# Performance work log

Hardware: AMD Instinct MI355X
Metric: run time of the kernel (lower is better)

Reference implementation:

```python
import jax, jax.numpy as jnp
import numpy as np
import math

B, S, D, H = 2, 2048, 1024, 16
HD = D // H  # head dim = 64


def setup_inputs() -> dict:
    key = jax.random.key(0)
    ks = jax.random.split(key, 8)
    scale = 1.0 / math.sqrt(D)
    return {
        "x": jax.random.normal(ks[0], (B, S, D), dtype=jnp.float32),
        "mask": jax.random.randint(ks[1], (B, S, S), 0, 2).astype(bool),
        "Wq": jax.random.normal(ks[2], (D, D), dtype=jnp.float32) * scale,
        "bq": jax.random.normal(ks[3], (D,), dtype=jnp.float32) * 0.01,
        "Wk": jax.random.normal(ks[4], (D, D), dtype=jnp.float32) * scale,
        "bk": jax.random.normal(ks[5], (D,), dtype=jnp.float32) * 0.01,
        "Wv": jax.random.normal(ks[6], (D, D), dtype=jnp.float32) * scale,
        "bv": jax.random.normal(ks[7], (D,), dtype=jnp.float32) * 0.01,
    }


def reference(x, mask, Wq, bq, Wk, bk, Wv, bv):
    # Linear projections (weights stored as [in, out])
    q = x @ Wq + bq  # [B,S,D]
    k = x @ Wk + bk
    v = x @ Wv + bv
    # split heads -> [B,H,S,HD]
    q = q.reshape(B, S, H, HD).transpose(0, 2, 1, 3)
    k = k.reshape(B, S, H, HD).transpose(0, 2, 1, 3)
    v = v.reshape(B, S, H, HD).transpose(0, 2, 1, 3)
    scores = jnp.einsum("bhqd,bhkd->bhqk", q, k) / jnp.sqrt(jnp.float32(HD))
    # Faithful to the source: masked_fill_(mask, -inf) is immediately
    # overwritten by masked_fill_(mask, 0), so masked positions end up 0
    # BEFORE the softmax (a quirk of the original module).
    scores = jnp.where(mask[:, None, :, :], 0.0, scores)
    attn = jax.nn.softmax(scores, axis=-1)  # dropout=0.0 (eval)
    out = jnp.einsum("bhqk,bhkd->bhqd", attn, v)
    return out.transpose(0, 2, 1, 3).reshape(B, S, D)
```

## Files before the change

kernel.cpp:

```cpp
#include <hip/hip_runtime.h>
#include <cstdint>
#include <cstddef>

static constexpr int B_ = 2, S_ = 2048, D_ = 1024, H_ = 16, HD_ = 64;

typedef float f32x4 __attribute__((ext_vector_type(4)));
typedef short bf16x8 __attribute__((ext_vector_type(8)));

__device__ __forceinline__ unsigned short f2bf(float f) {
    union { float f; unsigned int u; } v; v.f = f;
    unsigned int r = v.u + 0x7FFFu + ((v.u >> 16) & 1u);
    return (unsigned short)(r >> 16);
}
__device__ __forceinline__ float bf2f(unsigned short h) {
    union { unsigned int u; float f; } v; v.u = ((unsigned int)h) << 16;
    return v.f;
}

__global__ __launch_bounds__(256)
void cast_x(const float* __restrict__ x, unsigned short* __restrict__ o) {
    size_t i = ((size_t)blockIdx.x * 256 + threadIdx.x) * 8;
    float4 a = *(const float4*)(x + i);
    float4 c = *(const float4*)(x + i + 4);
    uint4 r;
    r.x = (unsigned)f2bf(a.x) | ((unsigned)f2bf(a.y) << 16);
    r.y = (unsigned)f2bf(a.z) | ((unsigned)f2bf(a.w) << 16);
    r.z = (unsigned)f2bf(c.x) | ((unsigned)f2bf(c.y) << 16);
    r.w = (unsigned)f2bf(c.z) | ((unsigned)f2bf(c.w) << 16);
    *(uint4*)(o + i) = r;
}

__global__ __launch_bounds__(256)
void transpose_w(const float* __restrict__ Wq, const float* __restrict__ Wk,
                 const float* __restrict__ Wv, unsigned short* __restrict__ wt) {
    const int mat = blockIdx.z;
    const float* __restrict__ W = (mat == 0) ? Wq : (mat == 1) ? Wk : Wv;
    unsigned short* __restrict__ o = wt + (size_t)mat * D_ * D_;
    const int n0 = blockIdx.x * 64, k0 = blockIdx.y * 64;
    __shared__ unsigned short Ts[64][72];
    const int t = threadIdx.x;
    {
        const int nl = t & 63, kb = t >> 6;
        #pragma unroll
        for (int i = 0; i < 16; ++i) {
            int k = kb + i * 4;
            Ts[nl][k] = f2bf(W[(size_t)(k0 + k) * D_ + n0 + nl]);
        }
    }
    __syncthreads();
    {
        const int kl = t & 63, nb = t >> 6;
        #pragma unroll
        for (int i = 0; i < 16; ++i) {
            int n = nb + i * 4;
            o[(size_t)(n0 + n) * D_ + k0 + kl] = Ts[n][kl];
        }
    }
}

__global__ __launch_bounds__(256)
void qkv_gemm(const unsigned short* __restrict__ xb, const unsigned short* __restrict__ wt,
              const float* __restrict__ bq, const float* __restrict__ bk,
              const float* __restrict__ bv,
              unsigned short* __restrict__ qo, unsigned short* __restrict__ ko,
              unsigned short* __restrict__ vo) {
    const int bx = blockIdx.x;
    const int by = blockIdx.y;
    const int mat = bx >> 3;
    const int ncol0 = (bx & 7) * 128;
    const float* __restrict__ bias = (mat == 0) ? bq : (mat == 1) ? bk : bv;
    unsigned short* __restrict__ O = (mat == 0) ? qo : (mat == 1) ? ko : vo;
    const unsigned short* __restrict__ Wm = wt + (size_t)mat * D_ * D_;

    __shared__ unsigned short As[128][40];
    __shared__ unsigned short Bs[128][40];

    const int t = threadIdx.x;
    const int w = t >> 6, lane = t & 63;
    const int l15 = lane & 15, quad = lane >> 4;
    const int mw = (w >> 1) * 64, nw = (w & 1) * 64;
    const int rowBase = by * 128;

    f32x4 acc[4][4] = {};

    for (int kt = 0; kt < D_; kt += 32) {
        __syncthreads();
        #pragma unroll
        for (int i = 0; i < 2; ++i) {
            int c = t + i * 256;
            int r = c >> 2, q = c & 3;
            *(uint4*)&As[r][q * 8] =
                *(const uint4*)(xb + (size_t)(rowBase + r) * D_ + kt + q * 8);
            *(uint4*)&Bs[r][q * 8] =
                *(const uint4*)(Wm + (size_t)(ncol0 + r) * D_ + kt + q * 8);
        }
        __syncthreads();

        bf16x8 a[4], b[4];
        #pragma unroll
        for (int i = 0; i < 4; ++i)
            a[i] = *(const bf16x8*)&As[mw + i * 16 + l15][quad * 8];
        #pragma unroll
        for (int j = 0; j < 4; ++j)
            b[j] = *(const bf16x8*)&Bs[nw + j * 16 + l15][quad * 8];
        #pragma unroll
        for (int i = 0; i < 4; ++i)
            #pragma unroll
            for (int j = 0; j < 4; ++j)
                acc[i][j] = __builtin_amdgcn_mfma_f32_16x16x32_bf16(a[i], b[j], acc[i][j], 0, 0, 0);
    }

    #pragma unroll
    for (int j = 0; j < 4; ++j) {
        const int col = ncol0 + nw + j * 16 + l15;
        const float bb = bias[col];
        #pragma unroll
        for (int i = 0; i < 4; ++i) {
            #pragma unroll
            for (int r = 0; r < 4; ++r) {
                const int m = rowBase + mw + i * 16 + quad * 4 + r;
                O[(size_t)m * D_ + col] = f2bf(acc[i][j][r] + bb);
            }
        }
    }
}

__global__ __launch_bounds__(256)
void attn_mfma(const unsigned short* __restrict__ qmat,
               const unsigned short* __restrict__ kmat,
               const unsigned short* __restrict__ vmat,
               const int* __restrict__ mask, float* __restrict__ out) {
    const int h = blockIdx.x, qt = blockIdx.y, b = blockIdx.z;
    const int t = threadIdx.x, w = t >> 6, lane = t & 63;
    const int l15 = lane & 15, quad = lane >> 4;
    const int q0 = qt * 128;

    __shared__ unsigned short Qs[128][72];
    __shared__ unsigned short Ks[64][72];
    __shared__ unsigned short Vt[64][72];
    __shared__ unsigned short Ps[128][72];

    const size_t bh = (size_t)b * S_ * D_ + (size_t)h * HD_;
    const unsigned short* __restrict__ qp = qmat + bh;
    const unsigned short* __restrict__ kp = kmat + bh;
    const unsigned short* __restrict__ vp = vmat + bh;
    const int* __restrict__ mb = mask + (size_t)b * S_ * S_;

    #pragma unroll
    for (int i = 0; i < 4; ++i) {
        int c = t + i * 256;
        int r = c >> 3, q8 = c & 7;
        *(uint4*)&Qs[r][q8 * 8] = *(const uint4*)(qp + (size_t)(q0 + r) * D_ + q8 * 8);
    }

    f32x4 accO[2][4] = {};
    float lsum[2][4] = {};

    for (int kt = 0; kt < S_; kt += 64) {
        __syncthreads();
        #pragma unroll
        for (int i = 0; i < 2; ++i) {
            int c = t + i * 256;
            int r = c >> 3, q8 = c & 7;
            *(uint4*)&Ks[r][q8 * 8] = *(const uint4*)(kp + (size_t)(kt + r) * D_ + q8 * 8);
        }
        {
            const int s = t & 63, d0 = (t >> 6) * 16;
            #pragma unroll
            for (int half = 0; half < 2; ++half) {
                uint4 v = *(const uint4*)(vp + (size_t)(kt + s) * D_ + d0 + half * 8);
                const unsigned short* pv = (const unsigned short*)&v;
                #pragma unroll
                for (int j = 0; j < 8; ++j) Vt[d0 + half * 8 + j][s] = pv[j];
            }
        }
        __syncthreads();

        f32x4 sc[2][4] = {};
        #pragma unroll
        for (int kst = 0; kst < 2; ++kst) {
            bf16x8 bfr[4];
            #pragma unroll
            for (int nt = 0; nt < 4; ++nt)
                bfr[nt] = *(const bf16x8*)&Ks[nt * 16 + l15][kst * 32 + quad * 8];
            #pragma unroll
            for (int mt = 0; mt < 2; ++mt) {
                bf16x8 afr = *(const bf16x8*)&Qs[w * 32 + mt * 16 + l15][kst * 32 + quad * 8];
                #pragma unroll
                for (int nt = 0; nt < 4; ++nt)
                    sc[mt][nt] = __builtin_amdgcn_mfma_f32_16x16x32_bf16(afr, bfr[nt], sc[mt][nt], 0, 0, 0);
            }
        }

        #pragma unroll
        for (int mt = 0; mt < 2; ++mt) {
            #pragma unroll
            for (int r = 0; r < 4; ++r) {
                const int lrow = w * 32 + mt * 16 + quad * 4 + r;
                const int* __restrict__ mr = mb + (size_t)(q0 + lrow) * S_ + kt;
                float ls = 0.f;
                #pragma unroll
                for (int nt = 0; nt < 4; ++nt) {
                    const int cc = nt * 16 + l15;
                    float s = sc[mt][nt][r] * 0.125f;
                    float p = (mr[cc] != 0) ? 1.0f : __expf(s);
                    unsigned short pb = f2bf(p);
                    Ps[lrow][cc] = pb;
                    ls += bf2f(pb);
                }
                lsum[mt][r] += ls;
            }
        }

        #pragma unroll
        for (int kst = 0; kst < 2; ++kst) {
            bf16x8 bfr[4];
            #pragma unroll
            for (int dt = 0; dt < 4; ++dt)
                bfr[dt] = *(const bf16x8*)&Vt[dt * 16 + l15][kst * 32 + quad * 8];
            #pragma unroll
            for (int mt = 0; mt < 2; ++mt) {
                bf16x8 afr = *(const bf16x8*)&Ps[w * 32 + mt * 16 + l15][kst * 32 + quad * 8];
                #pragma unroll
                for (int dt = 0; dt < 4; ++dt)
                    accO[mt][dt] = __builtin_amdgcn_mfma_f32_16x16x32_bf16(afr, bfr[dt], accO[mt][dt], 0, 0, 0);
            }
        }
    }

    float* __restrict__ ob = out + ((size_t)b * S_ + q0) * D_ + (size_t)h * HD_;
    #pragma unroll
    for (int mt = 0; mt < 2; ++mt) {
        #pragma unroll
        for (int r = 0; r < 4; ++r) {
            float v = lsum[mt][r];
            v += __shfl_xor(v, 1);
            v += __shfl_xor(v, 2);
            v += __shfl_xor(v, 4);
            v += __shfl_xor(v, 8);
            const float inv = 1.0f / v;
            const int lrow = w * 32 + mt * 16 + quad * 4 + r;
            #pragma unroll
            for (int dt = 0; dt < 4; ++dt)
                ob[(size_t)lrow * D_ + dt * 16 + l15] = accO[mt][dt][r] * inv;
        }
    }
}

extern "C" void kernel_launch(void* const* d_in, const int* in_sizes, int n_in,
                              void* d_out, int out_size, void* d_ws, size_t ws_size,
                              hipStream_t stream) {
    (void)in_sizes; (void)n_in; (void)out_size; (void)ws_size;
    const float* x    = (const float*)d_in[0];
    const int*   mask = (const int*)d_in[1];
    const float* Wq   = (const float*)d_in[2];
    const float* bq   = (const float*)d_in[3];
    const float* Wk   = (const float*)d_in[4];
    const float* bk   = (const float*)d_in[5];
    const float* Wv   = (const float*)d_in[6];
    const float* bv   = (const float*)d_in[7];
    float* out = (float*)d_out;

    unsigned short* xb = (unsigned short*)d_ws;
    unsigned short* wt = xb + (size_t)4 * 1024 * 1024;
    unsigned short* qb = wt + (size_t)3 * 1024 * 1024;
    unsigned short* kb = qb + (size_t)4 * 1024 * 1024;
    unsigned short* vb = kb + (size_t)4 * 1024 * 1024;

    cast_x<<<2048, 256, 0, stream>>>(x, xb);
    transpose_w<<<dim3(16, 16, 3), 256, 0, stream>>>(Wq, Wk, Wv, wt);
    qkv_gemm<<<dim3(24, 32), 256, 0, stream>>>(xb, wt, bq, bk, bv, qb, kb, vb);
    attn_mfma<<<dim3(16, 16, 2), 256, 0, stream>>>(qb, kb, vb, mask, out);
}
```

Baseline: 248.7 us.

## Pack mask to bytes, pre-transpose V, fold softmax scale into Q, MFMA rowsums

```diff
diff --git a/kernel.cpp b/kernel.cpp
--- a/kernel.cpp
+++ b/kernel.cpp
@@ -1,4 +1,5 @@
 #include <hip/hip_runtime.h>
+#include <hip/hip_bf16.h>
 #include <cstdint>
 #include <cstddef>
 
@@ -12,9 +13,15 @@
     unsigned int r = v.u + 0x7FFFu + ((v.u >> 16) & 1u);
     return (unsigned short)(r >> 16);
 }
-__device__ __forceinline__ float bf2f(unsigned short h) {
-    union { unsigned int u; float f; } v; v.u = ((unsigned int)h) << 16;
-    return v.f;
+
+__device__ __forceinline__ unsigned pack2bf(float a, float b) {
+#if __has_builtin(__builtin_amdgcn_cvt_pk_bf16_f32)
+    auto p = __builtin_amdgcn_cvt_pk_bf16_f32(a, b);
+    unsigned u; __builtin_memcpy(&u, &p, 4);
+    return u;
+#else
+    return (unsigned)f2bf(a) | ((unsigned)f2bf(b) << 16);
+#endif
 }
 
 __global__ __launch_bounds__(256)
@@ -23,10 +30,25 @@
     float4 a = *(const float4*)(x + i);
     float4 c = *(const float4*)(x + i + 4);
     uint4 r;
-    r.x = (unsigned)f2bf(a.x) | ((unsigned)f2bf(a.y) << 16);
-    r.y = (unsigned)f2bf(a.z) | ((unsigned)f2bf(a.w) << 16);
-    r.z = (unsigned)f2bf(c.x) | ((unsigned)f2bf(c.y) << 16);
-    r.w = (unsigned)f2bf(c.z) | ((unsigned)f2bf(c.w) << 16);
+    r.x = pack2bf(a.x, a.y);
+    r.y = pack2bf(a.z, a.w);
+    r.z = pack2bf(c.x, c.y);
+    r.w = pack2bf(c.z, c.w);
+    *(uint4*)(o + i) = r;
+}
+
+__global__ __launch_bounds__(256)
+void mask_pack(const int* __restrict__ m, unsigned char* __restrict__ o) {
+    size_t i = ((size_t)blockIdx.x * 256 + threadIdx.x) * 16;
+    uint4 r;
+    unsigned w[4];
+    #pragma unroll
+    for (int g = 0; g < 4; ++g) {
+        int4 v = *(const int4*)(m + i + g * 4);
+        w[g] = (v.x ? 1u : 0u) | (v.y ? 1u << 8 : 0u) |
+               (v.z ? 1u << 16 : 0u) | (v.w ? 1u << 24 : 0u);
+    }
+    r.x = w[0]; r.y = w[1]; r.z = w[2]; r.w = w[3];
     *(uint4*)(o + i) = r;
 }
 
@@ -63,13 +85,12 @@
               const float* __restrict__ bq, const float* __restrict__ bk,
               const float* __restrict__ bv,
               unsigned short* __restrict__ qo, unsigned short* __restrict__ ko,
-              unsigned short* __restrict__ vo) {
+              unsigned short* __restrict__ vto) {
     const int bx = blockIdx.x;
     const int by = blockIdx.y;
     const int mat = bx >> 3;
     const int ncol0 = (bx & 7) * 128;
     const float* __restrict__ bias = (mat == 0) ? bq : (mat == 1) ? bk : bv;
-    unsigned short* __restrict__ O = (mat == 0) ? qo : (mat == 1) ? ko : vo;
     const unsigned short* __restrict__ Wm = wt + (size_t)mat * D_ * D_;
 
     __shared__ unsigned short As[128][40];
@@ -110,17 +131,36 @@
                 acc[i][j] = __builtin_amdgcn_mfma_f32_16x16x32_bf16(a[i], b[j], acc[i][j], 0, 0, 0);
     }
 
-    #pragma unroll
-    for (int j = 0; j < 4; ++j) {
-        const int col = ncol0 + nw + j * 16 + l15;
-        const float bb = bias[col];
-        #pragma unroll
-        for (int i = 0; i < 4; ++i) {
-            #pragma unroll
-            for (int r = 0; r < 4; ++r) {
-                const int m = rowBase + mw + i * 16 + quad * 4 + r;
-                O[(size_t)m * D_ + col] = f2bf(acc[i][j][r] + bb);
-            }
+    if (mat < 2) {
+        unsigned short* __restrict__ O = (mat == 0) ? qo : ko;
+        const float osc = (mat == 0) ? 0.18033688011112443f : 1.0f;
+        #pragma unroll
+        for (int j = 0; j < 4; ++j) {
+            const int col = ncol0 + nw + j * 16 + l15;
+            const float bb = bias[col];
+            #pragma unroll
+            for (int i = 0; i < 4; ++i)
+                #pragma unroll
+                for (int r = 0; r < 4; ++r) {
+                    const int m = rowBase + mw + i * 16 + quad * 4 + r;
+                    O[(size_t)m * D_ + col] = f2bf((acc[i][j][r] + bb) * osc);
+                }
+        }
+    } else {
+        #pragma unroll
+        for (int j = 0; j < 4; ++j) {
+            const int col = ncol0 + nw + j * 16 + l15;
+            const float bb = bias[col];
+            const int hh = col >> 6, hd = col & 63;
+            #pragma unroll
+            for (int i = 0; i < 4; ++i)
+                #pragma unroll
+                for (int r = 0; r < 4; ++r) {
+                    const int m = rowBase + mw + i * 16 + quad * 4 + r;
+                    const int bg = m >> 11, s = m & 2047;
+                    vto[(((size_t)bg * H_ + hh) * HD_ + hd) * S_ + s] =
+                        f2bf(acc[i][j][r] + bb);
+                }
         }
     }
 }
@@ -128,123 +168,113 @@
 __global__ __launch_bounds__(256)
 void attn_mfma(const unsigned short* __restrict__ qmat,
                const unsigned short* __restrict__ kmat,
-               const unsigned short* __restrict__ vmat,
-               const int* __restrict__ mask, float* __restrict__ out) {
+               const unsigned short* __restrict__ vtg,
+               const unsigned char* __restrict__ msk, float* __restrict__ out) {
     const int h = blockIdx.x, qt = blockIdx.y, b = blockIdx.z;
     const int t = threadIdx.x, w = t >> 6, lane = t & 63;
     const int l15 = lane & 15, quad = lane >> 4;
     const int q0 = qt * 128;
 
-    __shared__ unsigned short Qs[128][72];
-    __shared__ unsigned short Ks[64][72];
-    __shared__ unsigned short Vt[64][72];
-    __shared__ unsigned short Ps[128][72];
+    __shared__ __align__(16) unsigned short Qs[128][72];
+    __shared__ __align__(16) unsigned short Ks[64][72];
+    __shared__ __align__(16) unsigned short Vt[64][72];
+    __shared__ __align__(16) unsigned short Ps[128][72];
 
     const size_t bh = (size_t)b * S_ * D_ + (size_t)h * HD_;
     const unsigned short* __restrict__ qp = qmat + bh;
     const unsigned short* __restrict__ kp = kmat + bh;
-    const unsigned short* __restrict__ vp = vmat + bh;
-    const int* __restrict__ mb = mask + (size_t)b * S_ * S_;
+    const unsigned short* __restrict__ vp = vtg + ((size_t)b * H_ + h) * HD_ * S_;
+    const unsigned char* __restrict__ mb = msk + (size_t)b * S_ * S_;
 
     #pragma unroll
-    for (int i = 0; i < 4; ++i) {
+    for (int i = 0; i < 2; ++i) {
         int c = t + i * 256;
-        int r = c >> 3, q8 = c & 7;
-        *(uint4*)&Qs[r][q8 * 8] = *(const uint4*)(qp + (size_t)(q0 + r) * D_ + q8 * 8);
+        int r = c >> 2, cg = (c & 3) * 16;
+        *(uint4*)&Qs[r][cg]     = *(const uint4*)(qp + (size_t)(q0 + r) * D_ + cg);
+        *(uint4*)&Qs[r][cg + 8] = *(const uint4*)(qp + (size_t)(q0 + r) * D_ + cg + 8);
     }
 
     f32x4 accO[2][4] = {};
-    float lsum[2][4] = {};
+    f32x4 lsA[2] = {};
+    bf16x8 ones;
+    #pragma unroll
+    for (int i = 0; i < 8; ++i) ones[i] = (short)0x3F80;
+
+    const int rstage = t >> 2, cstage = (t & 3) * 16;
 
     for (int kt = 0; kt < S_; kt += 64) {
         __syncthreads();
-        #pragma unroll
-        for (int i = 0; i < 2; ++i) {
-            int c = t + i * 256;
-            int r = c >> 3, q8 = c & 7;
-            *(uint4*)&Ks[r][q8 * 8] = *(const uint4*)(kp + (size_t)(kt + r) * D_ + q8 * 8);
-        }
-        {
-            const int s = t & 63, d0 = (t >> 6) * 16;
-            #pragma unroll
-            for (int half = 0; half < 2; ++half) {
-                uint4 v = *(const uint4*)(vp + (size_t)(kt + s) * D_ + d0 + half * 8);
-                const unsigned short* pv = (const unsigned short*)&v;
-                #pragma unroll
-                for (int j = 0; j < 8; ++j) Vt[d0 + half * 8 + j][s] = pv[j];
+        *(uint4*)&Ks[rstage][cstage]     = *(const uint4*)(kp + (size_t)(kt + rstage) * D_ + cstage);
+        *(uint4*)&Ks[rstage][cstage + 8] = *(const uint4*)(kp + (size_t)(kt + rstage) * D_ + cstage + 8);
+        *(uint4*)&Vt[rstage][cstage]     = *(const uint4*)(vp + (size_t)rstage * S_ + kt + cstage);
+        *(uint4*)&Vt[rstage][cstage + 8] = *(const uint4*)(vp + (size_t)rstage * S_ + kt + cstage + 8);
+        __syncthreads();
+
+        f32x4 sc[4][2] = {};
+        #pragma unroll
+        for (int kst = 0; kst < 2; ++kst) {
+            bf16x8 kfr[4], qfr[2];
+            #pragma unroll
+            for (int mt = 0; mt < 4; ++mt)
+                kfr[mt] = *(const bf16x8*)&Ks[mt * 16 + l15][kst * 32 + quad * 8];
+            #pragma unroll
+            for (int nt = 0; nt < 2; ++nt)
+                qfr[nt] = *(const bf16x8*)&Qs[w * 32 + nt * 16 + l15][kst * 32 + quad * 8];
+            #pragma unroll
+            for (int mt = 0; mt < 4; ++mt)
+                #pragma unroll
+                for (int nt = 0; nt < 2; ++nt)
+                    sc[mt][nt] = __builtin_amdgcn_mfma_f32_16x16x32_bf16(kfr[mt], qfr[nt], sc[mt][nt], 0, 0, 0);
+        }
+
+        #pragma unroll
+        for (int nt = 0; nt < 2; ++nt) {
+            const int qr = w * 32 + nt * 16 + l15;
+            const unsigned char* __restrict__ mrow = mb + (size_t)(q0 + qr) * S_ + kt;
+            #pragma unroll
+            for (int mt = 0; mt < 4; ++mt) {
+                const unsigned mu = *(const unsigned*)(mrow + mt * 16 + quad * 4);
+                float p[4];
+                #pragma unroll
+                for (int r = 0; r < 4; ++r) {
+                    float e = __builtin_amdgcn_exp2f(sc[mt][nt][r]);
+                    p[r] = ((mu >> (8 * r)) & 0xFFu) ? 1.0f : e;
+                }
+                uint2 pk;
+                pk.x = pack2bf(p[0], p[1]);
+                pk.y = pack2bf(p[2], p[3]);
+                *(uint2*)&Ps[qr][mt * 16 + quad * 4] = pk;
             }
         }
-        __syncthreads();
-
-        f32x4 sc[2][4] = {};
+
         #pragma unroll
         for (int kst = 0; kst < 2; ++kst) {
-            bf16x8 bfr[4];
-            #pragma unroll
-            for (int nt = 0; nt < 4; ++nt)
-                bfr[nt] = *(const bf16x8*)&Ks[nt * 16 + l15][kst * 32 + quad * 8];
+            bf16x8 vfr[4];
+            #pragma unroll
+            for (int dt = 0; dt < 4; ++dt)
+                vfr[dt] = *(const bf16x8*)&Vt[dt * 16 + l15][kst * 32 + quad * 8];
             #pragma unroll
             for (int mt = 0; mt < 2; ++mt) {
-                bf16x8 afr = *(const bf16x8*)&Qs[w * 32 + mt * 16 + l15][kst * 32 + quad * 8];
-                #pragma unroll
-                for (int nt = 0; nt < 4; ++nt)
-                    sc[mt][nt] = __builtin_amdgcn_mfma_f32_16x16x32_bf16(afr, bfr[nt], sc[mt][nt], 0, 0, 0);
-            }
-        }
-
-        #pragma unroll
-        for (int mt = 0; mt < 2; ++mt) {
-            #pragma unroll
-            for (int r = 0; r < 4; ++r) {
-                const int lrow = w * 32 + mt * 16 + quad * 4 + r;
-                const int* __restrict__ mr = mb + (size_t)(q0 + lrow) * S_ + kt;
-                float ls = 0.f;
-                #pragma unroll
-                for (int nt = 0; nt < 4; ++nt) {
-                    const int cc = nt * 16 + l15;
-                    float s = sc[mt][nt][r] * 0.125f;
-                    float p = (mr[cc] != 0) ? 1.0f : __expf(s);
-                    unsigned short pb = f2bf(p);
-                    Ps[lrow][cc] = pb;
-                    ls += bf2f(pb);
-                }
-                lsum[mt][r] += ls;
-            }
-        }
-
-        #pragma unroll
-        for (int kst = 0; kst < 2; ++kst) {
-            bf16x8 bfr[4];
-            #pragma unroll
-            for (int dt = 0; dt < 4; ++dt)
-                bfr[dt] = *(const bf16x8*)&Vt[dt * 16 + l15][kst * 32 + quad * 8];
-            #pragma unroll
-            for (int mt = 0; mt < 2; ++mt) {
-                bf16x8 afr = *(const bf16x8*)&Ps[w * 32 + mt * 16 + l15][kst * 32 + quad * 8];
+                bf16x8 pfr = *(const bf16x8*)&Ps[w * 32 + mt * 16 + l15][kst * 32 + quad * 8];
                 #pragma unroll
                 for (int dt = 0; dt < 4; ++dt)
-                    accO[mt][dt] = __builtin_amdgcn_mfma_f32_16x16x32_bf16(afr, bfr[dt], accO[mt][dt], 0, 0, 0);
+                    accO[mt][dt] = __builtin_amdgcn_mfma_f32_16x16x32_bf16(pfr, vfr[dt], accO[mt][dt], 0, 0, 0);
+                lsA[mt] = __builtin_amdgcn_mfma_f32_16x16x32_bf16(pfr, ones, lsA[mt], 0, 0, 0);
             }
         }
     }
 
     float* __restrict__ ob = out + ((size_t)b * S_ + q0) * D_ + (size_t)h * HD_;
     #pragma unroll
-    for (int mt = 0; mt < 2; ++mt) {
+    for (int mt = 0; mt < 2; ++mt)
         #pragma unroll
         for (int r = 0; r < 4; ++r) {
-            float v = lsum[mt][r];
-            v += __shfl_xor(v, 1);
-            v += __shfl_xor(v, 2);
-            v += __shfl_xor(v, 4);
-            v += __shfl_xor(v, 8);
-            const float inv = 1.0f / v;
-            const int lrow = w * 32 + mt * 16 + quad * 4 + r;
+            const float inv = 1.0f / lsA[mt][r];
+            const int qr = w * 32 + mt * 16 + quad * 4 + r;
             #pragma unroll
             for (int dt = 0; dt < 4; ++dt)
-                ob[(size_t)lrow * D_ + dt * 16 + l15] = accO[mt][dt][r] * inv;
-        }
-    }
+                ob[(size_t)qr * D_ + dt * 16 + l15] = accO[mt][dt][r] * inv;
+        }
 }
 
 extern "C" void kernel_launch(void* const* d_in, const int* in_sizes, int n_in,
@@ -261,14 +291,17 @@
     const float* bv   = (const float*)d_in[7];
     float* out = (float*)d_out;
 
-    unsigned short* xb = (unsigned short*)d_ws;
-    unsigned short* wt = xb + (size_t)4 * 1024 * 1024;
-    unsigned short* qb = wt + (size_t)3 * 1024 * 1024;
-    unsigned short* kb = qb + (size_t)4 * 1024 * 1024;
-    unsigned short* vb = kb + (size_t)4 * 1024 * 1024;
+    const size_t M1 = (size_t)1024 * 1024;
+    unsigned short* xb  = (unsigned short*)d_ws;
+    unsigned short* wtb = xb + 4 * M1;
+    unsigned short* qb  = wtb + 3 * M1;
+    unsigned short* kb  = qb + 4 * M1;
+    unsigned short* vtb = kb + 4 * M1;
+    unsigned char*  mk  = (unsigned char*)(vtb + 4 * M1);
 
     cast_x<<<2048, 256, 0, stream>>>(x, xb);
-    transpose_w<<<dim3(16, 16, 3), 256, 0, stream>>>(Wq, Wk, Wv, wt);
-    qkv_gemm<<<dim3(24, 32), 256, 0, stream>>>(xb, wt, bq, bk, bv, qb, kb, vb);
-    attn_mfma<<<dim3(16, 16, 2), 256, 0, stream>>>(qb, kb, vb, mask, out);
-}
+    mask_pack<<<2048, 256, 0, stream>>>(mask, mk);
+    transpose_w<<<dim3(16, 16, 3), 256, 0, stream>>>(Wq, Wk, Wv, wtb);
+    qkv_gemm<<<dim3(24, 32), 256, 0, stream>>>(xb, wtb, bq, bk, bv, qb, kb, vtb);
+    attn_mfma<<<dim3(16, 16, 2), 256, 0, stream>>>(qb, kb, vtb, mk, out);
+}
```

Result: slower. 256.6 us (+3.2%).
